# Kernel tuning notes

Measured on AMD Instinct MI355X. Metric: run time of the kernel, lower is better.

Reference implementation:

```python
import jax, jax.numpy as jnp
import numpy as np

H = 256          # hidden_dim
D = 64           # dim_dynamic
R = 49           # pooler_resolution ** 2
N = 2000         # bs * num_proposals
EPS = 1e-5


def _ln(x, g, b):
    m = jnp.mean(x, axis=-1, keepdims=True)
    v = jnp.mean(jnp.square(x - m), axis=-1, keepdims=True)
    return (x - m) * jax.lax.rsqrt(v + EPS) * g + b


def setup_inputs() -> dict:
    key = jax.random.key(0)
    ks = jax.random.split(key, 6)
    pro_features = jax.random.normal(ks[0], (1, N, H), dtype=jnp.float32)
    roi_features = jax.random.normal(ks[1], (R, N, H), dtype=jnp.float32)
    # dynamic_layer: Linear(H, num_dynamic * H * D) with num_dynamic = 2
    W_dyn = jax.random.normal(ks[2], (H, 2 * H * D), dtype=jnp.float32) * 0.02
    b_dyn = jnp.zeros((2 * H * D,), dtype=jnp.float32)
    # out_layer: Linear(H * R, H)
    W_out = jax.random.normal(ks[3], (H * R, H), dtype=jnp.float32) * 0.02
    b_out = jnp.zeros((H,), dtype=jnp.float32)
    g1 = jnp.ones((D,), dtype=jnp.float32); b1 = jnp.zeros((D,), dtype=jnp.float32)
    g2 = jnp.ones((H,), dtype=jnp.float32); b2 = jnp.zeros((H,), dtype=jnp.float32)
    g3 = jnp.ones((H,), dtype=jnp.float32); b3 = jnp.zeros((H,), dtype=jnp.float32)
    return {"pro_features": pro_features, "roi_features": roi_features,
            "W_dyn": W_dyn, "b_dyn": b_dyn, "W_out": W_out, "b_out": b_out,
            "g1": g1, "b1": b1, "g2": g2, "b2": b2, "g3": g3, "b3": b3}


def reference(pro_features, roi_features, W_dyn, b_dyn, W_out, b_out,
              g1, b1, g2, b2, g3, b3):
    # roi_features: (R, N, H) -> features: (N, R, H)
    feats = jnp.transpose(roi_features, (1, 0, 2))
    # per-instance dynamic parameters: (N, 2*H*D)
    params = pro_features[0] @ W_dyn + b_dyn
    num_params = H * D
    p1 = params[:, :num_params].reshape(-1, H, D)   # (N, H, D)
    p2 = params[:, num_params:].reshape(-1, D, H)   # (N, D, H)
    f = jnp.einsum('nrh,nhd->nrd', feats, p1)       # bmm 1
    f = jax.nn.relu(_ln(f, g1, b1))
    f = jnp.einsum('nrd,ndh->nrh', f, p2)           # bmm 2
    f = jax.nn.relu(_ln(f, g2, b2))
    f = f.reshape(f.shape[0], R * H)                # flatten(1)
    f = jax.nn.relu(_ln(f @ W_out + b_out, g3, b3))
    return f  # (N, H)
```

## Files before the change

### kernel.cpp

```cpp
#include <hip/hip_runtime.h>

typedef unsigned short u16;
typedef __attribute__((ext_vector_type(8))) short short8;
typedef __attribute__((ext_vector_type(4))) float f32x4;

#define N_INST 2000
#define H_DIM 256
#define D_DIM 64
#define R_DIM 49
#define LN_EPS 1e-5f
#define SPLITK 14

__device__ __forceinline__ u16 f2bf(float f) {
  union { float f; unsigned int i; } x; x.f = f;
  unsigned int r = x.i + 0x7fffu + ((x.i >> 16) & 1u);
  return (u16)(r >> 16);
}
__device__ __forceinline__ float bf2f(u16 u) {
  union { unsigned int i; float f; } x; x.i = ((unsigned int)u) << 16; return x.f;
}
__device__ __forceinline__ short8 ld8(const u16* p) {
  return *reinterpret_cast<const short8*>(p);
}
__device__ __forceinline__ short8 pack8(float4 a, float4 b) {
  short8 r;
  r[0] = (short)f2bf(a.x); r[1] = (short)f2bf(a.y);
  r[2] = (short)f2bf(a.z); r[3] = (short)f2bf(a.w);
  r[4] = (short)f2bf(b.x); r[5] = (short)f2bf(b.y);
  r[6] = (short)f2bf(b.z); r[7] = (short)f2bf(b.w);
  return r;
}
__device__ __forceinline__ f32x4 mfma16(short8 a, short8 b, f32x4 c) {
  return __builtin_amdgcn_mfma_f32_16x16x32_bf16(a, b, c, 0, 0, 0);
}
__device__ __forceinline__ void wave_reduce2(float& s, float& s2) {
#pragma unroll
  for (int off = 32; off > 0; off >>= 1) {
    s  += __shfl_down(s, off);
    s2 += __shfl_down(s2, off);
  }
  s = __shfl(s, 0); s2 = __shfl(s2, 0);
}
__device__ __forceinline__ void gload16(const u16* g, u16* l) {
  __builtin_amdgcn_global_load_lds(
      (const __attribute__((address_space(1))) void*)g,
      (__attribute__((address_space(3))) void*)l, 16, 0, 0);
}

__global__ __launch_bounds__(256) void cast_pro(const float* __restrict__ in,
                                                u16* __restrict__ out, int n4) {
  for (int i = blockIdx.x * 256 + threadIdx.x; i < n4; i += gridDim.x * 256) {
    float4 v = ((const float4*)in)[i];
    u16* op = out + i * 4;
    op[0] = f2bf(v.x); op[1] = f2bf(v.y); op[2] = f2bf(v.z); op[3] = f2bf(v.w);
  }
}

__global__ __launch_bounds__(256) void cast_wdyn(const float* __restrict__ W,
                                                 u16* __restrict__ WT, int half) {
  __shared__ u16 T[64][65];
  const int tid = threadIdx.x;
  const int wave = tid >> 6, lane = tid & 63;
  const int b = blockIdx.x;
  const int kt = b >> 8;
  long colbase, rowbase; int rstride;
  if (half == 0) {
    int h = b & 255;
    colbase = (long)h * 64; rowbase = h; rstride = 256;
  } else {
    int d = b & 63, hc = (b >> 6) & 3;
    colbase = 16384L + d * 256 + hc * 64;
    rowbase = 16384L + hc * 4096 + d; rstride = 64;
  }
#pragma unroll
  for (int i = 0; i < 16; ++i) {
    int kk = wave * 16 + i;
    int k = kt * 64 + kk;
    T[kk][lane] = f2bf(W[(long)k * 32768 + colbase + lane]);
  }
  __syncthreads();
#pragma unroll
  for (int i = 0; i < 16; ++i) {
    int jj = wave * 16 + i;
    long ro = rowbase + (long)jj * rstride;
    WT[ro * 256 + kt * 64 + lane] = T[lane][jj];
  }
}

__global__ __launch_bounds__(256) void cast_wout(const float* __restrict__ W,
                                                 u16* __restrict__ WT) {
  __shared__ u16 T[64][65];
  const int tid = threadIdx.x;
  const int wave = tid >> 6, lane = tid & 63;
  const int kt = blockIdx.x >> 2, ct = blockIdx.x & 3;
#pragma unroll
  for (int i = 0; i < 16; ++i) {
    int kk = wave * 16 + i;
    long k = (long)kt * 64 + kk;
    T[kk][lane] = f2bf(W[k * 256 + ct * 64 + lane]);
  }
  __syncthreads();
#pragma unroll
  for (int i = 0; i < 16; ++i) {
    int cc = wave * 16 + i;
    long c = (long)ct * 64 + cc;
    WT[c * 12544 + (long)kt * 64 + lane] = T[lane][cc];
  }
}

__global__ __launch_bounds__(256, 3) void gemm128(
    const u16* __restrict__ A, int lda, int M,
    const u16* __restrict__ BT, int ldbt,
    const float* __restrict__ bias, int bias_mode,
    void* __restrict__ Cout, int ldc, long c_stride_s,
    int ksteps, int n_blocks, int out_f32)
{
  union Smem {
    struct { u16 a[2][128 * 32]; u16 b[2][128 * 32]; } s;
    u16 cb[128 * 128];
  };
  __shared__ Smem sm;

  const int tid = threadIdx.x;
  const int wave = tid >> 6, lane = tid & 63;
  const int quad = lane >> 4, l16 = lane & 15;
  const int wm = wave >> 1, wn = wave & 1;
  const int bid = blockIdx.x;
  const int mblk = bid / n_blocks, nblk = bid - mblk * n_blocks;
  const int m0 = mblk * 128, n0 = nblk * 128;
  const int s = blockIdx.y;
  const int kb = s * ksteps * 32;

  const int cl = tid & 3;
  const int r0 = tid >> 2, r1 = 64 + (tid >> 2);
  const int cg0 = cl ^ ((r0 >> 1) & 3);
  const int cg1 = cl ^ ((r1 >> 1) & 3);
  int ga0 = m0 + r0; if (ga0 >= M) ga0 = M - 1;
  int ga1 = m0 + r1; if (ga1 >= M) ga1 = M - 1;
  const u16* gA0 = A + (long)ga0 * lda + kb + cg0 * 8;
  const u16* gA1 = A + (long)ga1 * lda + kb + cg1 * 8;
  const u16* gB0 = BT + (long)(n0 + r0) * ldbt + kb + cg0 * 8;
  const u16* gB1 = BT + (long)(n0 + r1) * ldbt + kb + cg1 * 8;

  int fAoff[4], fBoff[4];
#pragma unroll
  for (int i = 0; i < 4; ++i) {
    int rt = wm * 64 + i * 16 + l16;
    fAoff[i] = rt * 32 + (quad ^ ((rt >> 1) & 3)) * 8;
    int ct = wn * 64 + i * 16 + l16;
    fBoff[i] = ct * 32 + (quad ^ ((ct >> 1) & 3)) * 8;
  }

  f32x4 acc[4][4];
#pragma unroll
  for (int mi = 0; mi < 4; ++mi)
#pragma unroll
    for (int ni = 0; ni < 4; ++ni) acc[mi][ni] = f32x4{0.f, 0.f, 0.f, 0.f};

  gload16(gA0, &sm.s.a[0][tid * 8]);
  gload16(gA1, &sm.s.a[0][(tid + 256) * 8]);
  gload16(gB0, &sm.s.b[0][tid * 8]);
  gload16(gB1, &sm.s.b[0][(tid + 256) * 8]);

  for (int ks = 0; ks < ksteps; ++ks) {
    const int cur = ks & 1, nxt = cur ^ 1;
    __syncthreads();
    if (ks + 1 < ksteps) {
      const int ko = (ks + 1) * 32;
      gload16(gA0 + ko, &sm.s.a[nxt][tid * 8]);
      gload16(gA1 + ko, &sm.s.a[nxt][(tid + 256) * 8]);
      gload16(gB0 + ko, &sm.s.b[nxt][tid * 8]);
      gload16(gB1 + ko, &sm.s.b[nxt][(tid + 256) * 8]);
    }
    short8 av[4], bv[4];
#pragma unroll
    for (int i = 0; i < 4; ++i) {
      av[i] = ld8(&sm.s.a[cur][fAoff[i]]);
      bv[i] = ld8(&sm.s.b[cur][fBoff[i]]);
    }
#pragma unroll
    for (int mi = 0; mi < 4; ++mi)
#pragma unroll
      for (int ni = 0; ni < 4; ++ni)
        acc[mi][ni] = mfma16(av[mi], bv[ni], acc[mi][ni]);
  }

  if (!out_f32) {
    float bvv[4];
#pragma unroll
    for (int ni = 0; ni < 4; ++ni) {
      int col = n0 + wn * 64 + ni * 16 + l16;
      int bi = col;
      if (bias_mode == 3)
        bi = (col < 16384) ? (((col & 255) << 6) + (col >> 8))
                           : (16384 + ((col & 63) << 8) + ((col >> 6) & 255));
      bvv[ni] = bias ? bias[bi] : 0.f;
    }
    __syncthreads();
#pragma unroll
    for (int mi = 0; mi < 4; ++mi)
#pragma unroll
      for (int ni = 0; ni < 4; ++ni)
#pragma unroll
        for (int i = 0; i < 4; ++i) {
          int row = wm * 64 + mi * 16 + quad * 4 + i;
          int col = wn * 64 + ni * 16 + l16;
          sm.cb[row * 128 + col] = f2bf(acc[mi][ni][i] + bvv[ni]);
        }
    __syncthreads();
    u16* Cp = (u16*)Cout;
#pragma unroll
    for (int j = 0; j < 8; ++j) {
      int lin = j * 2048 + tid * 8;
      int row = lin >> 7, col = lin & 127;
      int grow = m0 + row;
      if (grow < M)
        *reinterpret_cast<short8*>(Cp + (long)grow * ldc + n0 + col) =
            ld8(&sm.cb[lin]);
    }
  } else {
    float* Cp = (float*)Cout + (long)s * c_stride_s;
#pragma unroll
    for (int mi = 0; mi < 4; ++mi)
#pragma unroll
      for (int ni = 0; ni < 4; ++ni) {
        int col = n0 + wn * 64 + ni * 16 + l16;
#pragma unroll
        for (int i = 0; i < 4; ++i) {
          int row = m0 + wm * 64 + mi * 16 + quad * 4 + i;
          if (row < M) Cp[(long)row * ldc + col] = acc[mi][ni][i];
        }
      }
  }
}

__global__ __launch_bounds__(256, 3) void bmm12_ln(
    const float* __restrict__ roi,
    const u16* __restrict__ P12,
    const float* __restrict__ g1, const float* __restrict__ b1,
    const float* __restrict__ g2, const float* __restrict__ b2,
    u16* __restrict__ f2n)
{
  __shared__ u16 reg0[16384];
  __shared__ u16 f1buf[4096];
  const int n = blockIdx.x;
  const int tid = threadIdx.x;
  const int wave = tid >> 6, lane = tid & 63;
  const int quad = lane >> 4, l16 = lane & 15;
  const int wstripe = wave * 16;

  const u16* P1n = P12 + (long)n * 32768;
#pragma unroll
  for (int j = 0; j < 8; ++j) {
    int lc = j * 256 + tid;
    int d = lc >> 5, c = lc & 31;
    int cg = (c & 24) | ((c & 7) ^ (d & 7));
    gload16(P1n + d * 256 + cg * 8, &reg0[lc * 8]);
  }
  int r = wstripe + l16;
  int rr = (r < R_DIM) ? r : 0;
  const float* Arow = roi + ((long)rr * N_INST + n) * H_DIM + quad * 8;
  float4 rv[16];
#pragma unroll
  for (int ks = 0; ks < 8; ++ks) {
    rv[2 * ks]     = ((const float4*)(Arow + ks * 32))[0];
    rv[2 * ks + 1] = ((const float4*)(Arow + ks * 32))[1];
  }
  float gv1[4], bv1[4];
#pragma unroll
  for (int sub = 0; sub < 4; ++sub) {
    gv1[sub] = g1[sub * 16 + l16]; bv1[sub] = b1[sub * 16 + l16];
  }
  __syncthreads();

  short8 sa[8];
#pragma unroll
  for (int ks = 0; ks < 8; ++ks) sa[ks] = pack8(rv[2 * ks], rv[2 * ks + 1]);

  f32x4 acc1[4];
#pragma unroll
  for (int i = 0; i < 4; ++i) acc1[i] = f32x4{0.f, 0.f, 0.f, 0.f};
#pragma unroll
  for (int ks = 0; ks < 8; ++ks) {
#pragma unroll
    for (int sub = 0; sub < 4; ++sub) {
      int d = sub * 16 + l16;
      int q = ks * 4 + quad;
      int c = (q & 24) | ((q & 7) ^ (d & 7));
      acc1[sub] = mfma16(sa[ks], ld8(&reg0[d * 256 + c * 8]), acc1[sub]);
    }
  }
  __syncthreads();

  const u16* P2n = P12 + (long)n * 32768 + 16384;
#pragma unroll
  for (int j = 0; j < 8; ++j) {
    int lc = j * 256 + tid;
    int h = lc >> 3, c = lc & 7;
    gload16(P2n + h * 64 + (c ^ (h & 7)) * 8, &reg0[lc * 8]);
  }

  {
    float s1[4], s2[4];
#pragma unroll
    for (int i = 0; i < 4; ++i) {
      s1[i] = 0.f; s2[i] = 0.f;
#pragma unroll
      for (int sub = 0; sub < 4; ++sub) {
        float v = acc1[sub][i]; s1[i] += v; s2[i] += v * v;
      }
    }
#pragma unroll
    for (int m = 1; m < 16; m <<= 1)
#pragma unroll
      for (int i = 0; i < 4; ++i) {
        s1[i] += __shfl_xor(s1[i], m, 16);
        s2[i] += __shfl_xor(s2[i], m, 16);
      }
#pragma unroll
    for (int i = 0; i < 4; ++i) {
      float mean = s1[i] * (1.f / 64.f);
      float var = s2[i] * (1.f / 64.f) - mean * mean;
      float rs = rsqrtf(var + LN_EPS);
      int row = wstripe + quad * 4 + i;
#pragma unroll
      for (int sub = 0; sub < 4; ++sub) {
        float y = fmaxf((acc1[sub][i] - mean) * rs * gv1[sub] + bv1[sub], 0.f);
        int kc = (sub * 2 + (l16 >> 3)) ^ (row & 7);
        f1buf[row * 64 + kc * 8 + (l16 & 7)] = f2bf(y);
      }
    }
  }
  __syncthreads();

  short8 af2[2];
#pragma unroll
  for (int ks = 0; ks < 2; ++ks) {
    int row = wstripe + l16;
    int c2 = (ks * 4 + quad) ^ (row & 7);
    af2[ks] = ld8(&f1buf[row * 64 + c2 * 8]);
  }
  f32x4 acc2[16];
#pragma unroll
  for (int i = 0; i < 16; ++i) acc2[i] = f32x4{0.f, 0.f, 0.f, 0.f};
#pragma unroll
  for (int ks = 0; ks < 2; ++ks) {
#pragma unroll
    for (int sub = 0; sub < 16; ++sub) {
      int h = sub * 16 + l16;
      int c = (ks * 4 + quad) ^ (h & 7);
      acc2[sub] = mfma16(af2[ks], ld8(&reg0[h * 64 + c * 8]), acc2[sub]);
    }
  }

  float mean2[4], rs2[4];
  {
    float s1[4], s2[4];
#pragma unroll
    for (int i = 0; i < 4; ++i) {
      s1[i] = 0.f; s2[i] = 0.f;
#pragma unroll
      for (int sub = 0; sub < 16; ++sub) {
        float v = acc2[sub][i]; s1[i] += v; s2[i] += v * v;
      }
    }
#pragma unroll
    for (int m = 1; m < 16; m <<= 1)
#pragma unroll
      for (int i = 0; i < 4; ++i) {
        s1[i] += __shfl_xor(s1[i], m, 16);
        s2[i] += __shfl_xor(s2[i], m, 16);
      }
#pragma unroll
    for (int i = 0; i < 4; ++i) {
      mean2[i] = s1[i] * (1.f / 256.f);
      float var = s2[i] * (1.f / 256.f) - mean2[i] * mean2[i];
      rs2[i] = rsqrtf(var + LN_EPS);
    }
  }
  __syncthreads();

#pragma unroll
  for (int i = 0; i < 4; ++i) {
    int row = wstripe + quad * 4 + i;
    if (row < R_DIM) {
#pragma unroll
      for (int sub = 0; sub < 16; ++sub)
        reg0[row * 264 + sub * 16 + l16] =
            f2bf((acc2[sub][i] - mean2[i]) * rs2[i]);
    }
  }
  __syncthreads();

  u16* f2out = f2n + (long)n * (R_DIM * H_DIM);
  for (int t = tid; t < R_DIM * 32; t += 256) {
    int row = t >> 5, c = t & 31;
    short8 z8 = ld8(&reg0[row * 264 + c * 8]);
    const float4* gp = (const float4*)(g2 + c * 8);
    const float4* bp = (const float4*)(b2 + c * 8);
    float4 ga = gp[0], gb = gp[1], ba = bp[0], bb = bp[1];
    short8 y;
    y[0] = (short)f2bf(fmaxf(bf2f((u16)z8[0]) * ga.x + ba.x, 0.f));
    y[1] = (short)f2bf(fmaxf(bf2f((u16)z8[1]) * ga.y + ba.y, 0.f));
    y[2] = (short)f2bf(fmaxf(bf2f((u16)z8[2]) * ga.z + ba.z, 0.f));
    y[3] = (short)f2bf(fmaxf(bf2f((u16)z8[3]) * ga.w + ba.w, 0.f));
    y[4] = (short)f2bf(fmaxf(bf2f((u16)z8[4]) * gb.x + bb.x, 0.f));
    y[5] = (short)f2bf(fmaxf(bf2f((u16)z8[5]) * gb.y + bb.y, 0.f));
    y[6] = (short)f2bf(fmaxf(bf2f((u16)z8[6]) * gb.z + bb.z, 0.f));
    y[7] = (short)f2bf(fmaxf(bf2f((u16)z8[7]) * gb.w + bb.w, 0.f));
    *reinterpret_cast<short8*>(f2out + row * 256 + c * 8) = y;
  }
}

__global__ __launch_bounds__(64) void ln3_k(
    const float* __restrict__ partial,
    const float* __restrict__ b_out,
    const float* __restrict__ g3, const float* __restrict__ b3,
    float* __restrict__ out)
{
  const int n = blockIdx.x;
  const int lane = threadIdx.x;
  float x[4], sv = 0.f, s2 = 0.f;
#pragma unroll
  for (int j = 0; j < 4; ++j) {
    int h = lane + 64 * j;
    float v = b_out[h];
#pragma unroll
    for (int ss = 0; ss < SPLITK; ++ss)
      v += partial[((long)ss * N_INST + n) * H_DIM + h];
    x[j] = v; sv += v; s2 += v * v;
  }
  wave_reduce2(sv, s2);
  float mean = sv * (1.f / 256.f);
  float var = s2 * (1.f / 256.f) - mean * mean;
  float rs = rsqrtf(var + LN_EPS);
#pragma unroll
  for (int j = 0; j < 4; ++j) {
    int h = lane + 64 * j;
    float y = fmaxf((x[j] - mean) * rs * g3[h] + b3[h], 0.f);
    out[(long)n * H_DIM + h] = y;
  }
}

extern "C" void kernel_launch(void* const* d_in, const int* in_sizes, int n_in,
                              void* d_out, int out_size, void* d_ws, size_t ws_size,
                              hipStream_t stream) {
  const float* pro  = (const float*)d_in[0];
  const float* roi  = (const float*)d_in[1];
  const float* Wdyn = (const float*)d_in[2];
  const float* bdyn = (const float*)d_in[3];
  const float* Wout = (const float*)d_in[4];
  const float* bout = (const float*)d_in[5];
  const float* g1 = (const float*)d_in[6];
  const float* b1 = (const float*)d_in[7];
  const float* g2 = (const float*)d_in[8];
  const float* b2 = (const float*)d_in[9];
  const float* g3 = (const float*)d_in[10];
  const float* b3 = (const float*)d_in[11];
  float* out = (float*)d_out;

  char* ws = (char*)d_ws;
  u16* proB  = (u16*)ws;
  u16* WdynT = (u16*)(ws + 1024000);
  u16* WoutT = (u16*)(ws + 17801216);
  u16* P12   = (u16*)(ws + 24223744);
  u16* f2n   = (u16*)(ws + 155295744);
  float* partial = (float*)(ws + 24223744);

  dim3 blk(256);

  cast_pro<<<dim3(500), blk, 0, stream>>>(pro, proB, 512000 / 4);
  cast_wdyn<<<dim3(1024), blk, 0, stream>>>(Wdyn, WdynT, 0);
  cast_wdyn<<<dim3(1024), blk, 0, stream>>>(Wdyn, WdynT, 1);
  cast_wout<<<dim3(784), blk, 0, stream>>>(Wout, WoutT);

  gemm128<<<dim3(16 * 256, 1), blk, 0, stream>>>(
      proB, H_DIM, N_INST, WdynT, H_DIM, bdyn, 3,
      (void*)P12, 32768, 0L, 8, 256, 0);
  bmm12_ln<<<dim3(N_INST), blk, 0, stream>>>(roi, P12, g1, b1, g2, b2, f2n);
  gemm128<<<dim3(16 * 2, SPLITK), blk, 0, stream>>>(
      f2n, R_DIM * H_DIM, N_INST, WoutT, R_DIM * H_DIM, nullptr, 0,
      (void*)partial, H_DIM, (long)N_INST * H_DIM, 28, 2, 1);
  ln3_k<<<dim3(N_INST), dim3(64), 0, stream>>>(partial, bout, g3, b3, out);
}
```

Baseline: 337.1 us.

## Store dynamic params in MFMA fragment order and drop LDS staging in bmm12

The parameter GEMM epilogue now writes P1/P2 per instance in a permuted layout that matches the MFMA B-fragment order. This lets bmm12_ln load B operands straight from global memory with coalesced 16-byte loads instead of staging them through LDS behind block barriers. Each wave now uses its own small LDS slice, so the block-wide syncs go away, LDS use drops, and the launch bound rises to 4 blocks. The two cast_wdyn launches are merged into one. In exchange, the P1/P2 operand reads go through L2/global instead of LDS.

```diff
diff --git a/kernel.cpp b/kernel.cpp
--- a/kernel.cpp
+++ b/kernel.cpp
@@ -57,11 +57,12 @@
 }
 
 __global__ __launch_bounds__(256) void cast_wdyn(const float* __restrict__ W,
-                                                 u16* __restrict__ WT, int half) {
+                                                 u16* __restrict__ WT) {
   __shared__ u16 T[64][65];
   const int tid = threadIdx.x;
   const int wave = tid >> 6, lane = tid & 63;
-  const int b = blockIdx.x;
+  const int half = blockIdx.x >> 10;
+  const int b = blockIdx.x & 1023;
   const int kt = b >> 8;
   long colbase, rowbase; int rstride;
   if (half == 0) {
@@ -111,9 +112,9 @@
 __global__ __launch_bounds__(256, 3) void gemm128(
     const u16* __restrict__ A, int lda, int M,
     const u16* __restrict__ BT, int ldbt,
-    const float* __restrict__ bias, int bias_mode,
+    const float* __restrict__ bias,
     void* __restrict__ Cout, int ldc, long c_stride_s,
-    int ksteps, int n_blocks, int out_f32)
+    int ksteps, int n_blocks, int cmode)
 {
   union Smem {
     struct { u16 a[2][128 * 32]; u16 b[2][128 * 32]; } s;
@@ -185,16 +186,14 @@
         acc[mi][ni] = mfma16(av[mi], bv[ni], acc[mi][ni]);
   }
 
-  if (!out_f32) {
+  if (cmode == 1) {
     float bvv[4];
 #pragma unroll
     for (int ni = 0; ni < 4; ++ni) {
       int col = n0 + wn * 64 + ni * 16 + l16;
-      int bi = col;
-      if (bias_mode == 3)
-        bi = (col < 16384) ? (((col & 255) << 6) + (col >> 8))
-                           : (16384 + ((col & 63) << 8) + ((col >> 6) & 255));
-      bvv[ni] = bias ? bias[bi] : 0.f;
+      int bi = (col < 16384) ? (((col & 255) << 6) + (col >> 8))
+                             : (16384 + ((col & 63) << 8) + ((col >> 6) & 255));
+      bvv[ni] = bias[bi];
     }
     __syncthreads();
 #pragma unroll
@@ -212,10 +211,21 @@
 #pragma unroll
     for (int j = 0; j < 8; ++j) {
       int lin = j * 2048 + tid * 8;
-      int row = lin >> 7, col = lin & 127;
+      int row = lin >> 7, col0 = n0 + (lin & 127);
       int grow = m0 + row;
+      long toff;
+      if (col0 < 16384) {
+        int d = col0 >> 8, h = col0 & 255;
+        toff = ((((d >> 4) * 8 + (h >> 5)) * 16 + (d & 15)) * 4 +
+                ((h >> 3) & 3)) * 8;
+      } else {
+        int c2 = col0 - 16384;
+        int h = c2 >> 6, d = c2 & 63;
+        toff = 16384 + ((((h >> 4) * 2 + (d >> 5)) * 16 + (h & 15)) * 4 +
+                        ((d >> 3) & 3)) * 8;
+      }
       if (grow < M)
-        *reinterpret_cast<short8*>(Cp + (long)grow * ldc + n0 + col) =
+        *reinterpret_cast<short8*>(Cp + (long)grow * 32768 + toff) =
             ld8(&sm.cb[lin]);
     }
   } else {
@@ -234,70 +244,46 @@
   }
 }
 
-__global__ __launch_bounds__(256, 3) void bmm12_ln(
+__global__ __launch_bounds__(256, 4) void bmm12_ln(
     const float* __restrict__ roi,
     const u16* __restrict__ P12,
     const float* __restrict__ g1, const float* __restrict__ b1,
     const float* __restrict__ g2, const float* __restrict__ b2,
     u16* __restrict__ f2n)
 {
-  __shared__ u16 reg0[16384];
-  __shared__ u16 f1buf[4096];
+  __shared__ u16 smem[4][16 * 264];
   const int n = blockIdx.x;
   const int tid = threadIdx.x;
   const int wave = tid >> 6, lane = tid & 63;
   const int quad = lane >> 4, l16 = lane & 15;
   const int wstripe = wave * 16;
-
-  const u16* P1n = P12 + (long)n * 32768;
-#pragma unroll
-  for (int j = 0; j < 8; ++j) {
-    int lc = j * 256 + tid;
-    int d = lc >> 5, c = lc & 31;
-    int cg = (c & 24) | ((c & 7) ^ (d & 7));
-    gload16(P1n + d * 256 + cg * 8, &reg0[lc * 8]);
-  }
+  u16* wsm = smem[wave];
+  const int lanebase = (l16 * 4 + quad) * 8;
+
+  const u16* P1f = P12 + (long)n * 32768;
+  const u16* P2f = P1f + 16384;
   int r = wstripe + l16;
   int rr = (r < R_DIM) ? r : 0;
   const float* Arow = roi + ((long)rr * N_INST + n) * H_DIM + quad * 8;
-  float4 rv[16];
-#pragma unroll
-  for (int ks = 0; ks < 8; ++ks) {
-    rv[2 * ks]     = ((const float4*)(Arow + ks * 32))[0];
-    rv[2 * ks + 1] = ((const float4*)(Arow + ks * 32))[1];
-  }
+
   float gv1[4], bv1[4];
 #pragma unroll
   for (int sub = 0; sub < 4; ++sub) {
     gv1[sub] = g1[sub * 16 + l16]; bv1[sub] = b1[sub * 16 + l16];
   }
-  __syncthreads();
-
-  short8 sa[8];
-#pragma unroll
-  for (int ks = 0; ks < 8; ++ks) sa[ks] = pack8(rv[2 * ks], rv[2 * ks + 1]);
 
   f32x4 acc1[4];
 #pragma unroll
   for (int i = 0; i < 4; ++i) acc1[i] = f32x4{0.f, 0.f, 0.f, 0.f};
 #pragma unroll
   for (int ks = 0; ks < 8; ++ks) {
+    const float4* ap = (const float4*)(Arow + ks * 32);
+    short8 af = pack8(ap[0], ap[1]);
 #pragma unroll
     for (int sub = 0; sub < 4; ++sub) {
-      int d = sub * 16 + l16;
-      int q = ks * 4 + quad;
-      int c = (q & 24) | ((q & 7) ^ (d & 7));
-      acc1[sub] = mfma16(sa[ks], ld8(&reg0[d * 256 + c * 8]), acc1[sub]);
-    }
-  }
-  __syncthreads();
-
-  const u16* P2n = P12 + (long)n * 32768 + 16384;
-#pragma unroll
-  for (int j = 0; j < 8; ++j) {
-    int lc = j * 256 + tid;
-    int h = lc >> 3, c = lc & 7;
-    gload16(P2n + h * 64 + (c ^ (h & 7)) * 8, &reg0[lc * 8]);
+      short8 bf = ld8(P1f + (sub * 8 + ks) * 512 + lanebase);
+      acc1[sub] = mfma16(af, bf, acc1[sub]);
+    }
   }
 
   {
@@ -322,36 +308,33 @@
       float mean = s1[i] * (1.f / 64.f);
       float var = s2[i] * (1.f / 64.f) - mean * mean;
       float rs = rsqrtf(var + LN_EPS);
-      int row = wstripe + quad * 4 + i;
+      int lrow = quad * 4 + i;
 #pragma unroll
       for (int sub = 0; sub < 4; ++sub) {
         float y = fmaxf((acc1[sub][i] - mean) * rs * gv1[sub] + bv1[sub], 0.f);
-        int kc = (sub * 2 + (l16 >> 3)) ^ (row & 7);
-        f1buf[row * 64 + kc * 8 + (l16 & 7)] = f2bf(y);
-      }
-    }
-  }
-  __syncthreads();
+        int kc = (sub * 2 + (l16 >> 3)) ^ (lrow & 7);
+        wsm[lrow * 64 + kc * 8 + (l16 & 7)] = f2bf(y);
+      }
+    }
+  }
 
   short8 af2[2];
 #pragma unroll
   for (int ks = 0; ks < 2; ++ks) {
-    int row = wstripe + l16;
-    int c2 = (ks * 4 + quad) ^ (row & 7);
-    af2[ks] = ld8(&f1buf[row * 64 + c2 * 8]);
+    int lrow = l16;
+    int c2 = (ks * 4 + quad) ^ (lrow & 7);
+    af2[ks] = ld8(&wsm[lrow * 64 + c2 * 8]);
   }
   f32x4 acc2[16];
 #pragma unroll
   for (int i = 0; i < 16; ++i) acc2[i] = f32x4{0.f, 0.f, 0.f, 0.f};
 #pragma unroll
-  for (int ks = 0; ks < 2; ++ks) {
+  for (int ks = 0; ks < 2; ++ks)
 #pragma unroll
     for (int sub = 0; sub < 16; ++sub) {
-      int h = sub * 16 + l16;
-      int c = (ks * 4 + quad) ^ (h & 7);
-      acc2[sub] = mfma16(af2[ks], ld8(&reg0[h * 64 + c * 8]), acc2[sub]);
-    }
-  }
+      short8 bf = ld8(P2f + (sub * 2 + ks) * 512 + lanebase);
+      acc2[sub] = mfma16(af2[ks], bf, acc2[sub]);
+    }
 
   float mean2[4], rs2[4];
   {
@@ -378,37 +361,38 @@
       rs2[i] = rsqrtf(var + LN_EPS);
     }
   }
-  __syncthreads();
 
 #pragma unroll
   for (int i = 0; i < 4; ++i) {
-    int row = wstripe + quad * 4 + i;
-    if (row < R_DIM) {
+    int lrow = quad * 4 + i;
+    if (wstripe + lrow < R_DIM) {
 #pragma unroll
       for (int sub = 0; sub < 16; ++sub)
-        reg0[row * 264 + sub * 16 + l16] =
+        wsm[lrow * 264 + sub * 16 + l16] =
             f2bf((acc2[sub][i] - mean2[i]) * rs2[i]);
     }
   }
-  __syncthreads();
 
   u16* f2out = f2n + (long)n * (R_DIM * H_DIM);
-  for (int t = tid; t < R_DIM * 32; t += 256) {
-    int row = t >> 5, c = t & 31;
-    short8 z8 = ld8(&reg0[row * 264 + c * 8]);
-    const float4* gp = (const float4*)(g2 + c * 8);
-    const float4* bp = (const float4*)(b2 + c * 8);
-    float4 ga = gp[0], gb = gp[1], ba = bp[0], bb = bp[1];
-    short8 y;
-    y[0] = (short)f2bf(fmaxf(bf2f((u16)z8[0]) * ga.x + ba.x, 0.f));
-    y[1] = (short)f2bf(fmaxf(bf2f((u16)z8[1]) * ga.y + ba.y, 0.f));
-    y[2] = (short)f2bf(fmaxf(bf2f((u16)z8[2]) * ga.z + ba.z, 0.f));
-    y[3] = (short)f2bf(fmaxf(bf2f((u16)z8[3]) * ga.w + ba.w, 0.f));
-    y[4] = (short)f2bf(fmaxf(bf2f((u16)z8[4]) * gb.x + bb.x, 0.f));
-    y[5] = (short)f2bf(fmaxf(bf2f((u16)z8[5]) * gb.y + bb.y, 0.f));
-    y[6] = (short)f2bf(fmaxf(bf2f((u16)z8[6]) * gb.z + bb.z, 0.f));
-    y[7] = (short)f2bf(fmaxf(bf2f((u16)z8[7]) * gb.w + bb.w, 0.f));
-    *reinterpret_cast<short8*>(f2out + row * 256 + c * 8) = y;
+  for (int t = lane; t < 16 * 32; t += 64) {
+    int lrow = t >> 5, c = t & 31;
+    int grow = wstripe + lrow;
+    if (grow < R_DIM) {
+      short8 z8 = ld8(&wsm[lrow * 264 + c * 8]);
+      const float4* gp = (const float4*)(g2 + c * 8);
+      const float4* bp = (const float4*)(b2 + c * 8);
+      float4 ga = gp[0], gb = gp[1], ba = bp[0], bb = bp[1];
+      short8 y;
+      y[0] = (short)f2bf(fmaxf(bf2f((u16)z8[0]) * ga.x + ba.x, 0.f));
+      y[1] = (short)f2bf(fmaxf(bf2f((u16)z8[1]) * ga.y + ba.y, 0.f));
+      y[2] = (short)f2bf(fmaxf(bf2f((u16)z8[2]) * ga.z + ba.z, 0.f));
+      y[3] = (short)f2bf(fmaxf(bf2f((u16)z8[3]) * ga.w + ba.w, 0.f));
+      y[4] = (short)f2bf(fmaxf(bf2f((u16)z8[4]) * gb.x + bb.x, 0.f));
+      y[5] = (short)f2bf(fmaxf(bf2f((u16)z8[5]) * gb.y + bb.y, 0.f));
+      y[6] = (short)f2bf(fmaxf(bf2f((u16)z8[6]) * gb.z + bb.z, 0.f));
+      y[7] = (short)f2bf(fmaxf(bf2f((u16)z8[7]) * gb.w + bb.w, 0.f));
+      *reinterpret_cast<short8*>(f2out + grow * 256 + c * 8) = y;
+    }
   }
 }
 
@@ -470,16 +454,15 @@
   dim3 blk(256);
 
   cast_pro<<<dim3(500), blk, 0, stream>>>(pro, proB, 512000 / 4);
-  cast_wdyn<<<dim3(1024), blk, 0, stream>>>(Wdyn, WdynT, 0);
-  cast_wdyn<<<dim3(1024), blk, 0, stream>>>(Wdyn, WdynT, 1);
+  cast_wdyn<<<dim3(2048), blk, 0, stream>>>(Wdyn, WdynT);
   cast_wout<<<dim3(784), blk, 0, stream>>>(Wout, WoutT);
 
   gemm128<<<dim3(16 * 256, 1), blk, 0, stream>>>(
-      proB, H_DIM, N_INST, WdynT, H_DIM, bdyn, 3,
-      (void*)P12, 32768, 0L, 8, 256, 0);
+      proB, H_DIM, N_INST, WdynT, H_DIM, bdyn,
+      (void*)P12, 32768, 0L, 8, 256, 1);
   bmm12_ln<<<dim3(N_INST), blk, 0, stream>>>(roi, P12, g1, b1, g2, b2, f2n);
   gemm128<<<dim3(16 * 2, SPLITK), blk, 0, stream>>>(
-      f2n, R_DIM * H_DIM, N_INST, WoutT, R_DIM * H_DIM, nullptr, 0,
-      (void*)partial, H_DIM, (long)N_INST * H_DIM, 28, 2, 1);
+      f2n, R_DIM * H_DIM, N_INST, WoutT, R_DIM * H_DIM, nullptr,
+      (void*)partial, H_DIM, (long)N_INST * H_DIM, 28, 2, 2);
   ln3_k<<<dim3(N_INST), dim3(64), 0, stream>>>(partial, bout, g3, b3, out);
 }
```

After: 344.3 us. 2.1% more time.
